# Kernel tuning notes

Hardware: AMD Instinct MI355X
Metric: run time of the kernel (lower is better)

## Reference

```python
import jax, jax.numpy as jnp
import numpy as np

B, S, D, DC, H = 4, 2048, 768, 384, 12
HD = DC // H  # compressed head_dim = 32


def setup_inputs() -> dict:
    key = jax.random.key(0)
    ks = jax.random.split(key, 8)
    std = 0.02
    return {
        "hidden_states": jax.random.normal(ks[0], (B, S, D), dtype=jnp.float32),
        "W_attn": jax.random.normal(ks[1], (D, 3 * D), dtype=jnp.float32) * std,
        "b_attn": jnp.zeros((3 * D,), dtype=jnp.float32),
        "P_q": jax.random.normal(ks[2], (D, DC), dtype=jnp.float32) * std,
        "P_k": jax.random.normal(ks[3], (D, DC), dtype=jnp.float32) * std,
        "P_v": jax.random.normal(ks[4], (D, DC), dtype=jnp.float32) * std,
        "W_back": jax.random.normal(ks[5], (DC, D), dtype=jnp.float32) * std,
        "W_proj": jax.random.normal(ks[6], (D, D), dtype=jnp.float32) * std,
        "b_proj": jnp.zeros((D,), dtype=jnp.float32),
    }


def reference(hidden_states, W_attn, b_attn, P_q, P_k, P_v, W_back, W_proj, b_proj):
    b, s, _ = hidden_states.shape
    # GPT-2 Conv1D style c_attn: out = x @ W + b, then split into q,k,v
    qkv = hidden_states @ W_attn + b_attn          # [B,S,3D]
    q, k, v = jnp.split(qkv, 3, axis=-1)           # each [B,S,D]
    # sparsify hooks: per-token linear compression D -> DC
    q = q @ P_q                                    # [B,S,DC]
    k = k @ P_k
    v = v @ P_v
    # split heads -> [B,H,S,HD]
    split = lambda t: t.reshape(b, s, H, HD).transpose(0, 2, 1, 3)
    qh, kh, vh = split(q), split(k), split(v)
    # naive attention with explicit causal mask (as in original _attn)
    scores = jnp.einsum("bhqd,bhkd->bhqk", qh, kh) / jnp.sqrt(jnp.float32(HD))
    causal = jnp.tril(jnp.ones((s, s), dtype=scores.dtype))  # [S,S]
    scores = scores * causal + (-10000.0) * (1.0 - causal)
    weights = jax.nn.softmax(scores, axis=-1)
    ctx = jnp.einsum("bhqk,bhkd->bhqd", weights, vh)         # [B,H,S,HD]
    # merge heads -> [B,S,DC]
    ctx = ctx.transpose(0, 2, 1, 3).reshape(b, s, DC)
    # backproject DC -> D, then c_proj
    out = ctx @ W_back                             # [B,S,D]
    out = out @ W_proj + b_proj                    # [B,S,D]
    return out
```

## Files before the change

kernel.cpp:

```cpp
#include <hip/hip_runtime.h>
#include <math.h>


typedef unsigned short u16;
typedef unsigned int   u32;

#define VLD 8320

using short8 = __attribute__((ext_vector_type(8))) short;
using bf16x4 = __attribute__((ext_vector_type(4))) short;
using f32x4  = __attribute__((ext_vector_type(4))) float;

__device__ __forceinline__ u16 f2bf(float f) {
  u32 u = __builtin_bit_cast(u32, f);
  u = (u + 0x7fffu + ((u >> 16) & 1u)) >> 16;
  return (u16)u;
}

__device__ __forceinline__ float b2f(u16 b) {
  return __builtin_bit_cast(float, (u32)b << 16);
}

__device__ __forceinline__ u32 cvtpk_bf16(float lo, float hi) {
  u32 d;
  asm("v_cvt_pk_bf16_f32 %0, %1, %2" : "=v"(d) : "v"(lo), "v"(hi));
  return d;
}

__device__ __forceinline__ bf16x4 pack4(const f32x4 v) {
  union { u32 u[2]; bf16x4 s; } c;
  c.u[0] = cvtpk_bf16(v[0], v[1]);
  c.u[1] = cvtpk_bf16(v[2], v[3]);
  return c.s;
}

__device__ __forceinline__ float exp2v(float x) {
  return __builtin_amdgcn_exp2f(x);
}

__device__ __forceinline__ f32x4 mfma16bf(bf16x4 a, bf16x4 b, f32x4 c) {
#if __has_builtin(__builtin_amdgcn_mfma_f32_16x16x16bf16_1k)
  return __builtin_amdgcn_mfma_f32_16x16x16bf16_1k(a, b, c, 0, 0, 0);
#elif __has_builtin(__builtin_amdgcn_mfma_f32_16x16x16_bf16)
  return __builtin_amdgcn_mfma_f32_16x16x16_bf16(a, b, c, 0, 0, 0);
#else
  f32x4 d;
  asm("v_mfma_f32_16x16x16_bf16 %0, %1, %2, %3"
      : "=v"(d) : "v"(a), "v"(b), "v"(c));
  return d;
#endif
}

__device__ __forceinline__ void gload_lds16(const void* g, void* l) {
  __builtin_amdgcn_global_load_lds((__attribute__((address_space(1))) u32*)g,
                                   (__attribute__((address_space(3))) u32*)l,
                                   16, 0, 0);
}

__global__ __launch_bounds__(256) void prep_all(
    const float* __restrict__ x, const float* __restrict__ Wa,
    const float* __restrict__ Wb, const float* __restrict__ Pq,
    const float* __restrict__ Pk, const float* __restrict__ Pv,
    const float* __restrict__ Wp,
    u16* __restrict__ x_bf, u16* __restrict__ Wat_bf, u16* __restrict__ Wbk_bf,
    u16* __restrict__ PT, u16* __restrict__ WprT) {
  __shared__ float t[32][33];
  const int blk = blockIdx.x, tid = threadIdx.x;
  if (blk < 8160) {
    const float* src; u16* dst; int i;
    if (blk < 6144)      { src = x;  dst = x_bf;   i = blk * 256 + tid; }
    else if (blk < 7872) { src = Wa; dst = Wat_bf; i = (blk - 6144) * 256 + tid; }
    else                 { src = Wb; dst = Wbk_bf; i = (blk - 7872) * 256 + tid; }
    const float4 v = ((const float4*)src)[i];
    ((ushort4*)dst)[i] = make_ushort4(f2bf(v.x), f2bf(v.y), f2bf(v.z), f2bf(v.w));
    return;
  }
  const float* src; u16* dst; int C, R, bx, by;
  if (blk < 8448)      { src = Pq; dst = PT;             R = 768; C = 384; int t2 = blk - 8160; bx = t2 % 12; by = t2 / 12; }
  else if (blk < 8736) { src = Pk; dst = PT + 384 * 768; R = 768; C = 384; int t2 = blk - 8448; bx = t2 % 12; by = t2 / 12; }
  else if (blk < 9024) { src = Pv; dst = PT + 768 * 768; R = 768; C = 384; int t2 = blk - 8736; bx = t2 % 12; by = t2 / 12; }
  else                 { src = Wp; dst = WprT;           R = 768; C = 768; int t2 = blk - 9024; bx = t2 % 24; by = t2 / 24; }
  const int c0 = bx * 32, r0 = by * 32, tx = tid & 31, ty = tid >> 5;
  for (int i = ty; i < 32; i += 8)
    t[i][tx] = src[(size_t)(r0 + i) * C + c0 + tx];
  __syncthreads();
  for (int i = ty; i < 32; i += 8)
    dst[(size_t)(c0 + i) * R + r0 + tx] = f2bf(t[tx][i]);
}

template<int OBF16>
__device__ __forceinline__ void gemm_tile(
    const u16* __restrict__ A, const u16* __restrict__ BT,
    const float* __restrict__ bias, void* __restrict__ Cv,
    int K, int lda, int ldb, int ldc, int m0, int n0, int biasmode, bool slab,
    u16* As, u16* Bs) {
  const int tid = threadIdx.x;
  const int l = tid & 63, w = tid >> 6;
  const int r = l & 15, g = l >> 4;
  const int koff = slab ? (m0 / 384) * 768 : 0;
  const u16* Ap = A + ((size_t)m0 + w * 16 + r) * lda + g * 8;
  const u16* Bp = BT + ((size_t)n0 + w * 16 + r) * ldb + koff + g * 8;
  f32x4 acc[4][4] = {};
  const int wma = (w >> 1) * 4, wnb = (w & 1) * 4;
  const int nk = K >> 5;

  auto stage = [&](int kt, int buf) {
    const int o = buf * 4096;
    gload_lds16(Ap + kt,                    &As[o + (size_t)tid * 8]);
    gload_lds16(Ap + kt + (size_t)64 * lda, &As[o + 2048 + (size_t)tid * 8]);
    gload_lds16(Bp + kt,                    &Bs[o + (size_t)tid * 8]);
    gload_lds16(Bp + kt + (size_t)64 * ldb, &Bs[o + 2048 + (size_t)tid * 8]);
  };

  stage(0, 0);
  stage(32, 1);
  int cur = 0;
  for (int t = 0; t < nk; ++t) {
    if (t + 1 < nk) asm volatile("s_waitcnt vmcnt(4)" ::: "memory");
    else            asm volatile("s_waitcnt vmcnt(0)" ::: "memory");
    __builtin_amdgcn_s_barrier();
    const int o = cur * 4096;
    short8 af[4], bfr[4];
    #pragma unroll
    for (int i = 0; i < 4; ++i) {
      af[i]  = *(const short8*)&As[o + ((wma + i) * 64 + l) * 8];
      bfr[i] = *(const short8*)&Bs[o + ((wnb + i) * 64 + l) * 8];
    }
    #pragma unroll
    for (int mi = 0; mi < 4; ++mi)
      #pragma unroll
      for (int ni = 0; ni < 4; ++ni)
        acc[mi][ni] = __builtin_amdgcn_mfma_f32_16x16x32_bf16(af[mi], bfr[ni],
                                                              acc[mi][ni], 0, 0, 0);
    asm volatile("s_waitcnt lgkmcnt(0)" ::: "memory");
    __builtin_amdgcn_s_barrier();
    if (t + 2 < nk) stage((t + 2) << 5, cur);
    cur ^= 1;
  }

  const int row0 = m0 + (w >> 1) * 64, col0 = n0 + (w & 1) * 64;
  #pragma unroll
  for (int ni = 0; ni < 4; ++ni) {
    const int col = col0 + ni * 16 + r;
    const float bvc = (biasmode == 1) ? bias[col] : 0.f;
    #pragma unroll
    for (int mi = 0; mi < 4; ++mi)
      #pragma unroll
      for (int j = 0; j < 4; ++j) {
        const int row = row0 + mi * 16 + 4 * g + j;
        float bv = bvc;
        if (biasmode == 2) bv = bias[row];
        const float v = acc[mi][ni][j] + bv;
        if (OBF16) ((u16*)Cv)[(size_t)row * ldc + col] = f2bf(v);
        else       ((float*)Cv)[(size_t)row * ldc + col] = v;
      }
  }
}

__global__ __launch_bounds__(256, 2) void gemm_prep(
    const u16* __restrict__ PT, const u16* __restrict__ Wat,
    const u16* __restrict__ WprT, const u16* __restrict__ Wbk,
    const float* __restrict__ ba,
    u16* __restrict__ WcT, u16* __restrict__ WbpT, float* __restrict__ bc) {
  __shared__ alignas(16) u16 As[8192], Bs[8192];
  const int t = blockIdx.x;
  if (t < 54) {
    gemm_tile<1>(PT, Wat, nullptr, WcT, 768, 768, 2304, 768,
                 (t % 9) * 128, (t / 9) * 128, 0, true, As, Bs);
  } else if (t < 72) {
    const int t2 = t - 54;
    gemm_tile<1>(WprT, Wbk, nullptr, WbpT, 768, 768, 768, 384,
                 (t2 % 6) * 128, (t2 / 6) * 128, 0, false, As, Bs);
  } else {
    const int c = (t - 72) * 144 + threadIdx.x;
    if (threadIdx.x < 144 && c < 1152) {
      const int slab = c / 384;
      const float* bs = ba + slab * 768;
      const u16* row = PT + (size_t)c * 768;
      float s = 0.f;
      for (int jj = 0; jj < 96; ++jj) {
        const short8 v = *(const short8*)&row[jj * 8];
        #pragma unroll
        for (int e = 0; e < 8; ++e)
          s = fmaf(bs[jj * 8 + e], b2f((u16)v[e]), s);
      }
      bc[c] = s;
    }
  }
}

__global__ __launch_bounds__(256, 2) void gemm_qkvt(
    const u16* __restrict__ x_bf, const u16* __restrict__ WcT,
    const float* __restrict__ bc, u16* __restrict__ QKbuf, u16* __restrict__ VTbuf) {
  __shared__ alignas(16) u16 As[8192], Bs[8192];
  const int t = blockIdx.x;
  const int w = (t & 7) * 72 + (t >> 3);
  const int s = w / 9, j = w % 9;
  if (j < 6) {
    gemm_tile<1>(x_bf, WcT, bc, QKbuf, 768, 768, 768, 768,
                 s * 128, j * 128, 1, false, As, Bs);
  } else {
    gemm_tile<1>(WcT + (size_t)768 * 768, x_bf, bc + 768, VTbuf, 768, 768, 768, VLD,
                 (j - 6) * 128, s * 128, 2, false, As, Bs);
  }
}

__global__ __launch_bounds__(256, 2) void gemm_out(
    const u16* __restrict__ ctx, const u16* __restrict__ WbpT,
    const float* __restrict__ bp, float* __restrict__ out) {
  __shared__ alignas(16) u16 As[8192], Bs[8192];
  const int t = blockIdx.x;
  const int w = (t & 7) * 48 + (t >> 3);
  gemm_tile<0>(ctx, WbpT, bp, out, 384, 384, 384, 768,
               (w / 6) * 128, (w % 6) * 128, 1, false, As, Bs);
}

__global__ __launch_bounds__(256, 4) void attn_kernel(
    const u16* __restrict__ QK, const u16* __restrict__ VT,
    u16* __restrict__ ctx) {
  __shared__ alignas(16) u16 Ks[2][2048];
  __shared__ alignas(16) u16 Vs[2][32 * 72];
  const int tid = threadIdx.x;
  const int w = tid >> 6, l = tid & 63;
  const int r = l & 15, g = l >> 4;
  const int idx = blockIdx.x;
  const int cc = 15 - idx / 48;
  const int bh = idx % 48;
  const int b = bh / 12, h = bh % 12;
  const size_t tok0 = (size_t)b * 2048;
  const int q0 = cc * 128 + w * 32;
  const u16* Qb = QK + (tok0 + q0) * 768 + h * 32;
  const u16* Kb = QK + tok0 * 768 + 384 + h * 32;
  const u16* Vb = VT + (size_t)(h * 32) * VLD + b * 2048;
  const float scale2 = 0.25500526474f;
  const float THR = 8.0f;
  const f32x4 fz = {0.f, 0.f, 0.f, 0.f};

  short8 qf[2];
  qf[0] = *(const short8*)&Qb[(size_t)r * 768 + 8 * g];
  qf[1] = *(const short8*)&Qb[(size_t)(16 + r) * 768 + 8 * g];

  float mrun[2] = {-3.0e38f, -3.0e38f};
  float lpart[2] = {0.f, 0.f};
  f32x4 o[2][2] = {};
  const int ntb = 2 * (cc + 1);
  const int ntw = (q0 + 31) / 64 + 1;

  const int krow = ((tid >> 6) << 4) + (tid & 15);
  const int kcol = ((tid >> 4) & 3) * 8;
  const int vd   = tid >> 3;
  const int vkc  = (tid & 7) * 8;

  uint4 vreg;
  auto stageK = [&](int t, int buf) {
    gload_lds16(&Kb[(size_t)(t * 64 + krow) * 768 + kcol], &Ks[buf][(size_t)tid * 8]);
  };
  auto loadV = [&](int t) {
    vreg = *(const uint4*)&Vb[(size_t)vd * VLD + t * 64 + vkc];
  };
  auto writeV = [&](int buf) {
    *(uint4*)&Vs[buf][vd * 72 + vkc] = vreg;
  };

  loadV(0); stageK(0, 0); writeV(0);
  __syncthreads();
  int cur = 0;
  for (int t = 0; t < ntb; ++t) {
    const bool pf = (t + 1 < ntb);
    if (pf) { loadV(t + 1); stageK(t + 1, cur ^ 1); }
    if (t < ntw) {
      short8 kf[4];
      #pragma unroll
      for (int kj = 0; kj < 4; ++kj)
        kf[kj] = *(const short8*)&Ks[cur][((kj * 64 + l)) * 8];
      bf16x4 vf[2][4];
      #pragma unroll
      for (int di = 0; di < 2; ++di)
        #pragma unroll
        for (int kj = 0; kj < 4; ++kj)
          vf[di][kj] = *(const bf16x4*)&Vs[cur][(16 * di + r) * 72 + kj * 16 + 4 * g];

      f32x4 s[2][4];
      __builtin_amdgcn_s_setprio(1);
      #pragma unroll
      for (int kj = 0; kj < 4; ++kj)
        #pragma unroll
        for (int mi = 0; mi < 2; ++mi)
          s[mi][kj] = __builtin_amdgcn_mfma_f32_16x16x32_bf16(kf[kj], qf[mi], fz, 0, 0, 0);
      __builtin_amdgcn_s_setprio(0);

      if (t == ntw - 1) {
        #pragma unroll
        for (int mi = 0; mi < 2; ++mi) {
          const int qq = q0 + mi * 16 + r;
          #pragma unroll
          for (int kj = 0; kj < 4; ++kj)
            #pragma unroll
            for (int jj = 0; jj < 4; ++jj) {
              const int kk = t * 64 + kj * 16 + 4 * g + jj;
              if (kk > qq) s[mi][kj][jj] = -3.0e38f;
            }
        }
      }

      #pragma unroll
      for (int mi = 0; mi < 2; ++mi) {
        const float a0 = fmaxf(fmaxf(s[mi][0][0], s[mi][0][1]), fmaxf(s[mi][0][2], s[mi][0][3]));
        const float a1 = fmaxf(fmaxf(s[mi][1][0], s[mi][1][1]), fmaxf(s[mi][1][2], s[mi][1][3]));
        const float a2 = fmaxf(fmaxf(s[mi][2][0], s[mi][2][1]), fmaxf(s[mi][2][2], s[mi][2][3]));
        const float a3 = fmaxf(fmaxf(s[mi][3][0], s[mi][3][1]), fmaxf(s[mi][3][2], s[mi][3][3]));
        const float lmxs = fmaxf(fmaxf(a0, a1), fmaxf(a2, a3)) * scale2;
        if (__any(lmxs > mrun[mi] + THR)) {
          float mx = lmxs;
          mx = fmaxf(mx, __shfl_xor(mx, 16));
          mx = fmaxf(mx, __shfl_xor(mx, 32));
          const float mnew = fmaxf(mrun[mi], mx);
          const float al = exp2v(mrun[mi] - mnew);
          mrun[mi] = mnew;
          lpart[mi] *= al;
          o[0][mi] *= al;
          o[1][mi] *= al;
        }
        #pragma unroll
        for (int kj = 0; kj < 4; ++kj)
          #pragma unroll
          for (int jj = 0; jj < 4; ++jj) {
            const float pv = exp2v(fmaf(s[mi][kj][jj], scale2, -mrun[mi]));
            s[mi][kj][jj] = pv;
            lpart[mi] += pv;
          }
      }

      __builtin_amdgcn_s_setprio(1);
      #pragma unroll
      for (int kj = 0; kj < 4; ++kj) {
        const bf16x4 pf0 = pack4(s[0][kj]);
        const bf16x4 pf1 = pack4(s[1][kj]);
        #pragma unroll
        for (int di = 0; di < 2; ++di) {
          o[di][0] = mfma16bf(vf[di][kj], pf0, o[di][0]);
          o[di][1] = mfma16bf(vf[di][kj], pf1, o[di][1]);
        }
      }
      __builtin_amdgcn_s_setprio(0);
    }
    if (pf) writeV(cur ^ 1);
    __syncthreads();
    cur ^= 1;
  }

  #pragma unroll
  for (int mi = 0; mi < 2; ++mi) {
    float lr = lpart[mi];
    lr += __shfl_xor(lr, 16);
    lr += __shfl_xor(lr, 32);
    const float li = 1.0f / lr;
    const size_t row = tok0 + q0 + mi * 16 + r;
    #pragma unroll
    for (int di = 0; di < 2; ++di) {
      const u32 d0 = cvtpk_bf16(o[di][mi][0] * li, o[di][mi][1] * li);
      const u32 d1 = cvtpk_bf16(o[di][mi][2] * li, o[di][mi][3] * li);
      *(uint2*)&ctx[row * 384 + h * 32 + di * 16 + 4 * g] = make_uint2(d0, d1);
    }
  }
}

extern "C" void kernel_launch(void* const* d_in, const int* in_sizes, int n_in,
                              void* d_out, int out_size, void* d_ws, size_t ws_size,
                              hipStream_t stream) {
  const float* x      = (const float*)d_in[0];
  const float* W_attn = (const float*)d_in[1];
  const float* b_attn = (const float*)d_in[2];
  const float* P_q    = (const float*)d_in[3];
  const float* P_k    = (const float*)d_in[4];
  const float* P_v    = (const float*)d_in[5];
  const float* W_back = (const float*)d_in[6];
  const float* W_proj = (const float*)d_in[7];
  const float* b_proj = (const float*)d_in[8];

  char* ws = (char*)d_ws;
  u16*   x_bf   = (u16*)(ws);
  u16*   ctx    = (u16*)(ws);
  u16*   Wat_bf = (u16*)(ws + 12582912);
  u16*   PT     = (u16*)(ws + 16121856);
  u16*   Wbk_bf = (u16*)(ws + 17891328);
  u16*   WprT   = (u16*)(ws + 18481152);
  u16*   WcT    = (u16*)(ws + 19660800);
  u16*   WbpT   = (u16*)(ws + 21430272);
  float* bc     = (float*)(ws + 22020096);
  u16*   QKbuf  = (u16*)d_out;
  u16*   VTbuf  = (u16*)((char*)d_out + 12582912);
  float* out    = (float*)d_out;

  prep_all<<<9600, 256, 0, stream>>>(x, W_attn, W_back, P_q, P_k, P_v, W_proj,
                                     x_bf, Wat_bf, Wbk_bf, PT, WprT);
  gemm_prep<<<80, 256, 0, stream>>>(PT, Wat_bf, WprT, Wbk_bf, b_attn, WcT, WbpT, bc);
  gemm_qkvt<<<576, 256, 0, stream>>>(x_bf, WcT, bc, QKbuf, VTbuf);
  attn_kernel<<<768, 256, 0, stream>>>(QKbuf, VTbuf, ctx);
  gemm_out<<<384, 256, 0, stream>>>(ctx, WbpT, b_proj, out);
}
```

Measured before the change: 127.1 us.

## Replace LDS-staged GEMM tiles with direct global-to-register double-buffered loads

The shared GEMM tile routine no longer stages A and B tiles through LDS with barriers. Each wave now loads its own MFMA operand fragments straight from global memory into registers, ping-ponging two register sets so the next k-slice loads while the current one feeds the MFMAs. This removes LDS traffic, waitcnt/barrier synchronisation and shared-memory allocation. In exchange, waves that share rows or columns load the same operands redundantly (each A/B fragment is fetched by two waves), which relies on L1/L2 to absorb the reuse, and register pressure rises.

```diff
diff --git a/kernel.cpp b/kernel.cpp
--- a/kernel.cpp
+++ b/kernel.cpp
@@ -92,50 +92,41 @@
 __device__ __forceinline__ void gemm_tile(
     const u16* __restrict__ A, const u16* __restrict__ BT,
     const float* __restrict__ bias, void* __restrict__ Cv,
-    int K, int lda, int ldb, int ldc, int m0, int n0, int biasmode, bool slab,
-    u16* As, u16* Bs) {
+    int K, int lda, int ldb, int ldc, int m0, int n0, int biasmode, bool slab) {
   const int tid = threadIdx.x;
   const int l = tid & 63, w = tid >> 6;
   const int r = l & 15, g = l >> 4;
   const int koff = slab ? (m0 / 384) * 768 : 0;
-  const u16* Ap = A + ((size_t)m0 + w * 16 + r) * lda + g * 8;
-  const u16* Bp = BT + ((size_t)n0 + w * 16 + r) * ldb + koff + g * 8;
+  const int wma = (w >> 1) * 4, wnb = (w & 1) * 4;
+  const u16* Ap = A + (size_t)(m0 + wma * 16 + r) * lda + g * 8;
+  const u16* Bp = BT + (size_t)(n0 + wnb * 16 + r) * ldb + koff + g * 8;
   f32x4 acc[4][4] = {};
-  const int wma = (w >> 1) * 4, wnb = (w & 1) * 4;
   const int nk = K >> 5;
 
-  auto stage = [&](int kt, int buf) {
-    const int o = buf * 4096;
-    gload_lds16(Ap + kt,                    &As[o + (size_t)tid * 8]);
-    gload_lds16(Ap + kt + (size_t)64 * lda, &As[o + 2048 + (size_t)tid * 8]);
-    gload_lds16(Bp + kt,                    &Bs[o + (size_t)tid * 8]);
-    gload_lds16(Bp + kt + (size_t)64 * ldb, &Bs[o + 2048 + (size_t)tid * 8]);
-  };
-
-  stage(0, 0);
-  stage(32, 1);
-  int cur = 0;
-  for (int t = 0; t < nk; ++t) {
-    if (t + 1 < nk) asm volatile("s_waitcnt vmcnt(4)" ::: "memory");
-    else            asm volatile("s_waitcnt vmcnt(0)" ::: "memory");
-    __builtin_amdgcn_s_barrier();
-    const int o = cur * 4096;
-    short8 af[4], bfr[4];
+  short8 a0[4], b0[4], a1[4], b1[4];
+
+  auto loadf = [&](short8 (&aa)[4], short8 (&bb)[4], int kt) {
     #pragma unroll
     for (int i = 0; i < 4; ++i) {
-      af[i]  = *(const short8*)&As[o + ((wma + i) * 64 + l) * 8];
-      bfr[i] = *(const short8*)&Bs[o + ((wnb + i) * 64 + l) * 8];
+      aa[i] = *(const short8*)(Ap + (size_t)(i * 16) * lda + kt);
+      bb[i] = *(const short8*)(Bp + (size_t)(i * 16) * ldb + kt);
     }
+  };
+  auto mfmaf = [&](short8 (&aa)[4], short8 (&bb)[4]) {
     #pragma unroll
     for (int mi = 0; mi < 4; ++mi)
       #pragma unroll
       for (int ni = 0; ni < 4; ++ni)
-        acc[mi][ni] = __builtin_amdgcn_mfma_f32_16x16x32_bf16(af[mi], bfr[ni],
+        acc[mi][ni] = __builtin_amdgcn_mfma_f32_16x16x32_bf16(aa[mi], bb[ni],
                                                               acc[mi][ni], 0, 0, 0);
-    asm volatile("s_waitcnt lgkmcnt(0)" ::: "memory");
-    __builtin_amdgcn_s_barrier();
-    if (t + 2 < nk) stage((t + 2) << 5, cur);
-    cur ^= 1;
+  };
+
+  loadf(a0, b0, 0);
+  for (int t = 0; t < nk; t += 2) {
+    loadf(a1, b1, (t + 1) * 32);
+    mfmaf(a0, b0);
+    if (t + 2 < nk) loadf(a0, b0, (t + 2) * 32);
+    mfmaf(a1, b1);
   }
 
   const int row0 = m0 + (w >> 1) * 64, col0 = n0 + (w & 1) * 64;
@@ -162,15 +153,14 @@
     const u16* __restrict__ WprT, const u16* __restrict__ Wbk,
     const float* __restrict__ ba,
     u16* __restrict__ WcT, u16* __restrict__ WbpT, float* __restrict__ bc) {
-  __shared__ alignas(16) u16 As[8192], Bs[8192];
   const int t = blockIdx.x;
   if (t < 54) {
     gemm_tile<1>(PT, Wat, nullptr, WcT, 768, 768, 2304, 768,
-                 (t % 9) * 128, (t / 9) * 128, 0, true, As, Bs);
+                 (t % 9) * 128, (t / 9) * 128, 0, true);
   } else if (t < 72) {
     const int t2 = t - 54;
     gemm_tile<1>(WprT, Wbk, nullptr, WbpT, 768, 768, 768, 384,
-                 (t2 % 6) * 128, (t2 / 6) * 128, 0, false, As, Bs);
+                 (t2 % 6) * 128, (t2 / 6) * 128, 0, false);
   } else {
     const int c = (t - 72) * 144 + threadIdx.x;
     if (threadIdx.x < 144 && c < 1152) {
@@ -192,27 +182,25 @@
 __global__ __launch_bounds__(256, 2) void gemm_qkvt(
     const u16* __restrict__ x_bf, const u16* __restrict__ WcT,
     const float* __restrict__ bc, u16* __restrict__ QKbuf, u16* __restrict__ VTbuf) {
-  __shared__ alignas(16) u16 As[8192], Bs[8192];
   const int t = blockIdx.x;
   const int w = (t & 7) * 72 + (t >> 3);
   const int s = w / 9, j = w % 9;
   if (j < 6) {
     gemm_tile<1>(x_bf, WcT, bc, QKbuf, 768, 768, 768, 768,
-                 s * 128, j * 128, 1, false, As, Bs);
+                 s * 128, j * 128, 1, false);
   } else {
     gemm_tile<1>(WcT + (size_t)768 * 768, x_bf, bc + 768, VTbuf, 768, 768, 768, VLD,
-                 (j - 6) * 128, s * 128, 2, false, As, Bs);
+                 (j - 6) * 128, s * 128, 2, false);
   }
 }
 
 __global__ __launch_bounds__(256, 2) void gemm_out(
     const u16* __restrict__ ctx, const u16* __restrict__ WbpT,
     const float* __restrict__ bp, float* __restrict__ out) {
-  __shared__ alignas(16) u16 As[8192], Bs[8192];
   const int t = blockIdx.x;
   const int w = (t & 7) * 48 + (t >> 3);
   gemm_tile<0>(ctx, WbpT, bp, out, 384, 384, 384, 768,
-               (w / 6) * 128, (w % 6) * 128, 1, false, As, Bs);
+               (w / 6) * 128, (w % 6) * 128, 1, false);
 }
 
 __global__ __launch_bounds__(256, 4) void attn_kernel(
@@ -386,7 +374,7 @@
   u16*   Wbk_bf = (u16*)(ws + 17891328);
   u16*   WprT   = (u16*)(ws + 18481152);
   u16*   WcT    = (u16*)(ws + 19660800);
-  u16*   WbpT   = (u16*)(ws + 21430272);
+  u16*   WbpT  = (u16*)(ws + 21430272);
   float* bc     = (float*)(ws + 22020096);
   u16*   QKbuf  = (u16*)d_out;
   u16*   VTbuf  = (u16*)((char*)d_out + 12582912);
```

New measurement: 174.9 us. 37.6% more time.
